# Optimization experiments

Hardware: AMD Instinct MI355X
Metric: run time of the kernel (lower is better)

## Reference

```python
import jax, jax.numpy as jnp
import numpy as np

B = 4096   # batch
I = 1024   # in_features
O = 1024   # out_features
N = 4      # LUT fan-in; table size 2**N = 16


def setup_inputs() -> dict:
    key = jax.random.key(0)
    k1, k2, k3 = jax.random.split(key, 3)
    return {
        "x": jax.random.normal(k1, (B, I), dtype=jnp.float32),
        # learnable mapping logits: (out_features, n, in_features)
        "mapping_logits": jax.random.normal(k2, (O, N, I), dtype=jnp.float32),
        # per-node LUT tables with 2**n corner values each
        "lut_tables": jax.random.normal(k3, (O, 2 ** N), dtype=jnp.float32),
    }


def reference(x, mapping_logits, lut_tables):
    # softmax-weighted input selection: (B,I) x (O,N,I) -> (B,O,N)
    w = jax.nn.softmax(mapping_logits, axis=-1)
    selected = jnp.einsum('bi,oni->bon', x, w)
    # BatchedLUTNodes: squash to [0,1], multilinear interpolation over 2**N corners
    s = jax.nn.sigmoid(selected)                      # (B,O,N)
    cw = jnp.ones(s.shape[:2] + (1,), dtype=s.dtype)  # corner weights, grows to (B,O,2**N)
    for j in range(N):                                # fixed small loop over fan-in
        sj = s[..., j][..., None]                     # (B,O,1)
        cw = jnp.concatenate([cw * (1.0 - sj), cw * sj], axis=-1)
    # weighted sum of per-node table entries -> (B,O)
    return jnp.einsum('boc,oc->bo', cw, lut_tables)
```

## Files before the change

kernel.cpp:

```cpp
#include <hip/hip_runtime.h>

#define B_DIM 4096
#define I_DIM 1024
#define O_DIM 1024
#define ON_DIM 4096
#define TILE_HALFS 4096

typedef _Float16 half8  __attribute__((ext_vector_type(8)));
typedef _Float16 half4_t __attribute__((ext_vector_type(4)));
typedef float    floatx4 __attribute__((ext_vector_type(4)));

__global__ __launch_bounds__(256)
void ltn_stats(const float* __restrict__ logits, float2* __restrict__ stats) {
  const int t = threadIdx.x, lane = t & 63, wv = t >> 6;
  const int row = blockIdx.x * 4 + wv;
  const float4* src = (const float4*)(logits + (size_t)row * I_DIM);
  float4 v[4];
#pragma unroll
  for (int j = 0; j < 4; j++) v[j] = src[j * 64 + lane];
  float m = -1e30f;
#pragma unroll
  for (int j = 0; j < 4; j++)
    m = fmaxf(m, fmaxf(fmaxf(v[j].x, v[j].y), fmaxf(v[j].z, v[j].w)));
#pragma unroll
  for (int off = 1; off < 64; off <<= 1) m = fmaxf(m, __shfl_xor(m, off));
  float s = 0.0f;
#pragma unroll
  for (int j = 0; j < 4; j++) {
    s += __expf(v[j].x - m) + __expf(v[j].y - m)
       + __expf(v[j].z - m) + __expf(v[j].w - m);
  }
#pragma unroll
  for (int off = 1; off < 64; off <<= 1) s += __shfl_xor(s, off);
  if (lane == 0) stats[row] = make_float2(m, 1.0f / s);
}

__global__ __launch_bounds__(256)
void ltn_tile(const float* __restrict__ logits, const float* __restrict__ x,
              const float2* __restrict__ stats,
              _Float16* __restrict__ wt, _Float16* __restrict__ xt) {
  const int t  = threadIdx.x;
  const int nn = t >> 1;
  const int hf = t & 1;
  if (blockIdx.x < 1024) {
    const int nb = blockIdx.x >> 5, kb = blockIdx.x & 31;
    const int row = nb * 128 + nn;
    const float2 st = stats[row];
    const float4* src = (const float4*)(logits + (size_t)row * I_DIM + kb * 32 + hf * 16);
    const float4 a = src[0], b = src[1], c = src[2], d = src[3];
    half8 h0, h1;
    h0[0] = (_Float16)(__expf(a.x - st.x) * st.y);
    h0[1] = (_Float16)(__expf(a.y - st.x) * st.y);
    h0[2] = (_Float16)(__expf(a.z - st.x) * st.y);
    h0[3] = (_Float16)(__expf(a.w - st.x) * st.y);
    h0[4] = (_Float16)(__expf(b.x - st.x) * st.y);
    h0[5] = (_Float16)(__expf(b.y - st.x) * st.y);
    h0[6] = (_Float16)(__expf(b.z - st.x) * st.y);
    h0[7] = (_Float16)(__expf(b.w - st.x) * st.y);
    h1[0] = (_Float16)(__expf(c.x - st.x) * st.y);
    h1[1] = (_Float16)(__expf(c.y - st.x) * st.y);
    h1[2] = (_Float16)(__expf(c.z - st.x) * st.y);
    h1[3] = (_Float16)(__expf(c.w - st.x) * st.y);
    h1[4] = (_Float16)(__expf(d.x - st.x) * st.y);
    h1[5] = (_Float16)(__expf(d.y - st.x) * st.y);
    h1[6] = (_Float16)(__expf(d.z - st.x) * st.y);
    h1[7] = (_Float16)(__expf(d.w - st.x) * st.y);
    _Float16* base = wt + ((size_t)nb * 32 + kb) * TILE_HALFS + (hf * 2) * 1024 + nn * 8;
    *(half8*)base = h0;
    *(half8*)(base + 1024) = h1;
  } else {
    const int bid = blockIdx.x - 1024;
    const int mb = bid >> 5, kt = bid & 31;
    const int row = mb * 128 + nn;
    const float4* src = (const float4*)(x + (size_t)row * I_DIM + kt * 32 + hf * 16);
    const float4 a = src[0], b = src[1], c = src[2], d = src[3];
    half8 h0, h1;
    h0[0] = (_Float16)a.x; h0[1] = (_Float16)a.y; h0[2] = (_Float16)a.z; h0[3] = (_Float16)a.w;
    h0[4] = (_Float16)b.x; h0[5] = (_Float16)b.y; h0[6] = (_Float16)b.z; h0[7] = (_Float16)b.w;
    h1[0] = (_Float16)c.x; h1[1] = (_Float16)c.y; h1[2] = (_Float16)c.z; h1[3] = (_Float16)c.w;
    h1[4] = (_Float16)d.x; h1[5] = (_Float16)d.y; h1[6] = (_Float16)d.z; h1[7] = (_Float16)d.w;
    _Float16* base = xt + ((size_t)mb * 32 + kt) * TILE_HALFS + (hf * 2) * 1024 + nn * 8;
    *(half8*)base = h0;
    *(half8*)(base + 1024) = h1;
  }
}

__global__ __launch_bounds__(512, 2)
void ltn_gemm_lut(const _Float16* __restrict__ xt,
                  const _Float16* __restrict__ wt,
                  const float* __restrict__ lut,
                  float* __restrict__ out) {
  __shared__ _Float16 As[2][2][4][128][8];
  __shared__ _Float16 Bs[2][2][4][128][8];

  const int tid  = threadIdx.x;
  const int lane = tid & 63;
  const int wv   = tid >> 6;
  const int wr   = wv >> 1;
  const int wc   = wv & 1;
  const int mb   = blockIdx.x;
  const int nb   = blockIdx.y;
  const int fm   = lane & 15;
  const int kq   = lane >> 4;

  const size_t baseA = (size_t)(mb * 2) * 32 * TILE_HALFS;
  const size_t baseB = (size_t)(nb * 2) * 32 * TILE_HALFS;

  floatx4 acc[4][8];
#pragma unroll
  for (int i = 0; i < 4; i++)
#pragma unroll
    for (int j = 0; j < 8; j++) acc[i][j] = (floatx4)0.0f;

  auto stage = [&](int buf, int kt) {
#pragma unroll
    for (int s = 0; s < 4; s++) {
      const int c   = wv * 4 + s;
      const int cc  = c & 15;
      const int tl  = cc >> 3;
      const int sub = cc & 7;
      const _Float16* g;
      char* l;
      if (c < 16) {
        g = xt + baseA + (size_t)(tl * 32 + kt) * TILE_HALFS + sub * 512 + lane * 8;
        l = (char*)&As[buf][0][0][0][0] + cc * 1024;
      } else {
        g = wt + baseB + (size_t)(tl * 32 + kt) * TILE_HALFS + sub * 512 + lane * 8;
        l = (char*)&Bs[buf][0][0][0][0] + cc * 1024;
      }
      __builtin_amdgcn_global_load_lds(
          (const __attribute__((address_space(1))) void*)g,
          (__attribute__((address_space(3))) void*)l, 16, 0, 0);
    }
  };

  auto compute = [&](int buf) {
    half8 af[4], bf[8];
#pragma unroll
    for (int f = 0; f < 4; f++)
      af[f] = *(const half8*)&As[buf][wr >> 1][kq][(wr & 1) * 64 + f * 16 + fm][0];
#pragma unroll
    for (int g = 0; g < 8; g++)
      bf[g] = *(const half8*)&Bs[buf][wc][kq][g * 16 + fm][0];
#pragma unroll
    for (int mt = 0; mt < 4; mt++)
#pragma unroll
      for (int nt = 0; nt < 8; nt++)
        acc[mt][nt] = __builtin_amdgcn_mfma_f32_16x16x32_f16(
            af[mt], bf[nt], acc[mt][nt], 0, 0, 0);
  };

  stage(0, 0);
  int buf = 0;
  for (int kt = 0; kt < 32; kt++) {
    __syncthreads();
    if (kt + 1 < 32) stage(buf ^ 1, kt + 1);
    compute(buf);
    buf ^= 1;
  }

#pragma unroll
  for (int nt = 0; nt < 8; nt++) {
    const int o = (nb * 256 + wc * 128 + nt * 16 + fm) >> 2;
    const float4* lt4 = (const float4*)(lut + (size_t)o * 16);
    const float4 L0 = lt4[0], L1 = lt4[1], L2 = lt4[2], L3 = lt4[3];
#pragma unroll
    for (int mt = 0; mt < 4; mt++) {
#pragma unroll
      for (int r = 0; r < 4; r++) {
        const float v  = acc[mt][nt][r];
        const float sv = 1.0f / (1.0f + __expf(-v));
        const float s1 = __shfl_down(sv, 1);
        const float s2 = __shfl_down(sv, 2);
        const float s3 = __shfl_down(sv, 3);
        if ((lane & 3) == 0) {
          const float s0 = sv;
          const float a0 = L0.x + (L2.x - L0.x) * s3;
          const float a1 = L0.y + (L2.y - L0.y) * s3;
          const float a2 = L0.z + (L2.z - L0.z) * s3;
          const float a3 = L0.w + (L2.w - L0.w) * s3;
          const float a4 = L1.x + (L3.x - L1.x) * s3;
          const float a5 = L1.y + (L3.y - L1.y) * s3;
          const float a6 = L1.z + (L3.z - L1.z) * s3;
          const float a7 = L1.w + (L3.w - L1.w) * s3;
          const float b0 = a0 + (a4 - a0) * s2;
          const float b1 = a1 + (a5 - a1) * s2;
          const float b2 = a2 + (a6 - a2) * s2;
          const float b3 = a3 + (a7 - a3) * s2;
          const float c0 = b0 + (b2 - b0) * s1;
          const float c1 = b1 + (b3 - b1) * s1;
          const float res = c0 + (c1 - c0) * s0;
          const int row = mb * 256 + wr * 64 + mt * 16 + (lane >> 4) * 4 + r;
          out[(size_t)row * O_DIM + o] = res;
        }
      }
    }
  }
}

extern "C" void kernel_launch(void* const* d_in, const int* in_sizes, int n_in,
                              void* d_out, int out_size, void* d_ws, size_t ws_size,
                              hipStream_t stream) {
  const float* x      = (const float*)d_in[0];
  const float* logits = (const float*)d_in[1];
  const float* lut    = (const float*)d_in[2];
  float* out          = (float*)d_out;

  _Float16* wt = (_Float16*)d_ws;
  _Float16* xt = (_Float16*)d_ws + (size_t)ON_DIM * I_DIM;
  float2* stats = (float2*)d_out;

  ltn_stats<<<1024, 256, 0, stream>>>(logits, stats);
  ltn_tile<<<2048, 256, 0, stream>>>(logits, x, stats, wt, xt);
  dim3 grid(16, 16);
  ltn_gemm_lut<<<grid, 512, 0, stream>>>(xt, wt, lut, out);
}
```

Before: 134.2 us.

## Triple-buffer GEMM LDS pipeline with vmcnt waits and XCD-aware block remap

```diff
diff --git a/kernel.cpp b/kernel.cpp
--- a/kernel.cpp
+++ b/kernel.cpp
@@ -90,18 +90,22 @@
                   const _Float16* __restrict__ wt,
                   const float* __restrict__ lut,
                   float* __restrict__ out) {
-  __shared__ _Float16 As[2][2][4][128][8];
-  __shared__ _Float16 Bs[2][2][4][128][8];
+  __shared__ _Float16 sm[3 * 16384];
 
   const int tid  = threadIdx.x;
   const int lane = tid & 63;
   const int wv   = tid >> 6;
   const int wr   = wv >> 1;
   const int wc   = wv & 1;
-  const int mb   = blockIdx.x;
-  const int nb   = blockIdx.y;
-  const int fm   = lane & 15;
-  const int kq   = lane >> 4;
+
+  const int id  = blockIdx.x;
+  const int xcd = id & 7;
+  const int li  = id >> 3;
+  const int mb  = (xcd & 3) * 4 + (li & 3);
+  const int nb  = (xcd >> 2) * 8 + (li >> 2);
+
+  const int fm = lane & 15;
+  const int kq = lane >> 4;
 
   const size_t baseA = (size_t)(mb * 2) * 32 * TILE_HALFS;
   const size_t baseB = (size_t)(nb * 2) * 32 * TILE_HALFS;
@@ -112,7 +116,7 @@
 #pragma unroll
     for (int j = 0; j < 8; j++) acc[i][j] = (floatx4)0.0f;
 
-  auto stage = [&](int buf, int kt) {
+  auto stage = [&](int bufOff , int kt) {
 #pragma unroll
     for (int s = 0; s < 4; s++) {
       const int c   = wv * 4 + s;
@@ -120,43 +124,52 @@
       const int tl  = cc >> 3;
       const int sub = cc & 7;
       const _Float16* g;
-      char* l;
+      int dst;
       if (c < 16) {
         g = xt + baseA + (size_t)(tl * 32 + kt) * TILE_HALFS + sub * 512 + lane * 8;
-        l = (char*)&As[buf][0][0][0][0] + cc * 1024;
+        dst = bufOff + cc * 512;
       } else {
         g = wt + baseB + (size_t)(tl * 32 + kt) * TILE_HALFS + sub * 512 + lane * 8;
-        l = (char*)&Bs[buf][0][0][0][0] + cc * 1024;
+        dst = bufOff + 8192 + cc * 512;
       }
       __builtin_amdgcn_global_load_lds(
           (const __attribute__((address_space(1))) void*)g,
-          (__attribute__((address_space(3))) void*)l, 16, 0, 0);
+          (__attribute__((address_space(3))) void*)(sm + dst), 16, 0, 0);
     }
   };
 
-  auto compute = [&](int buf) {
+  auto compute = [&](int bufOff) {
     half8 af[4], bf[8];
 #pragma unroll
     for (int f = 0; f < 4; f++)
-      af[f] = *(const half8*)&As[buf][wr >> 1][kq][(wr & 1) * 64 + f * 16 + fm][0];
+      af[f] = *(const half8*)&sm[bufOff + ((wr >> 1) * 4 + kq) * 1024
+                                 + ((wr & 1) * 64 + f * 16 + fm) * 8];
 #pragma unroll
     for (int g = 0; g < 8; g++)
-      bf[g] = *(const half8*)&Bs[buf][wc][kq][g * 16 + fm][0];
+      bf[g] = *(const half8*)&sm[bufOff + 8192 + (wc * 4 + kq) * 1024
+                                 + (g * 16 + fm) * 8];
+    __builtin_amdgcn_s_setprio(1);
 #pragma unroll
     for (int mt = 0; mt < 4; mt++)
 #pragma unroll
       for (int nt = 0; nt < 8; nt++)
         acc[mt][nt] = __builtin_amdgcn_mfma_f32_16x16x32_f16(
             af[mt], bf[nt], acc[mt][nt], 0, 0, 0);
+    __builtin_amdgcn_s_setprio(0);
   };
 
   stage(0, 0);
-  int buf = 0;
+  stage(16384, 1);
+  int o0 = 0, o1 = 16384, o2 = 32768;
+
   for (int kt = 0; kt < 32; kt++) {
-    __syncthreads();
-    if (kt + 1 < 32) stage(buf ^ 1, kt + 1);
-    compute(buf);
-    buf ^= 1;
+    if (kt < 31) asm volatile("s_waitcnt vmcnt(4)" ::: "memory");
+    else         asm volatile("s_waitcnt vmcnt(0)" ::: "memory");
+    __builtin_amdgcn_s_barrier();
+    __builtin_amdgcn_sched_barrier(0);
+    if (kt + 2 < 32) stage(o2, kt + 2);
+    compute(o0);
+    const int t0 = o0; o0 = o1; o1 = o2; o2 = t0;
   }
 
 #pragma unroll
@@ -212,6 +225,5 @@
 
   ltn_stats<<<1024, 256, 0, stream>>>(logits, stats);
   ltn_tile<<<2048, 256, 0, stream>>>(logits, x, stats, wt, xt);
-  dim3 grid(16, 16);
-  ltn_gemm_lut<<<grid, 512, 0, stream>>>(xt, wt, lut, out);
-}
+  ltn_gemm_lut<<<256, 512, 0, stream>>>(xt, wt, lut, out);
+}
```

After: 132.4 us. No clear change (-1.3%).

## Shrink GEMM block tile to 128x128 with XCD-aware block swizzle

Applied to the files above, without the earlier changes.

```diff
diff --git a/kernel.cpp b/kernel.cpp
--- a/kernel.cpp
+++ b/kernel.cpp
@@ -85,48 +85,50 @@
   }
 }
 
-__global__ __launch_bounds__(512, 2)
+__global__ __launch_bounds__(256, 4)
 void ltn_gemm_lut(const _Float16* __restrict__ xt,
                   const _Float16* __restrict__ wt,
                   const float* __restrict__ lut,
                   float* __restrict__ out) {
-  __shared__ _Float16 As[2][2][4][128][8];
-  __shared__ _Float16 Bs[2][2][4][128][8];
+  __shared__ _Float16 As[2][4][128][8];
+  __shared__ _Float16 Bs[2][4][128][8];
 
   const int tid  = threadIdx.x;
   const int lane = tid & 63;
   const int wv   = tid >> 6;
   const int wr   = wv >> 1;
   const int wc   = wv & 1;
-  const int mb   = blockIdx.x;
-  const int nb   = blockIdx.y;
-  const int fm   = lane & 15;
-  const int kq   = lane >> 4;
-
-  const size_t baseA = (size_t)(mb * 2) * 32 * TILE_HALFS;
-  const size_t baseB = (size_t)(nb * 2) * 32 * TILE_HALFS;
-
-  floatx4 acc[4][8];
+
+  const int id  = blockIdx.x;
+  const int xcd = id & 7;
+  const int li  = id >> 3;
+  const int mb  = (xcd & 3) * 8 + (li & 7);
+  const int nb  = (xcd >> 2) * 16 + (li >> 3);
+
+  const int fm = lane & 15;
+  const int kq = lane >> 4;
+
+  const size_t baseA = (size_t)mb * 32 * TILE_HALFS;
+  const size_t baseB = (size_t)nb * 32 * TILE_HALFS;
+
+  floatx4 acc[4][4];
 #pragma unroll
   for (int i = 0; i < 4; i++)
 #pragma unroll
-    for (int j = 0; j < 8; j++) acc[i][j] = (floatx4)0.0f;
+    for (int j = 0; j < 4; j++) acc[i][j] = (floatx4)0.0f;
 
   auto stage = [&](int buf, int kt) {
 #pragma unroll
     for (int s = 0; s < 4; s++) {
-      const int c   = wv * 4 + s;
-      const int cc  = c & 15;
-      const int tl  = cc >> 3;
-      const int sub = cc & 7;
+      const int c = wv * 4 + s;
       const _Float16* g;
       char* l;
-      if (c < 16) {
-        g = xt + baseA + (size_t)(tl * 32 + kt) * TILE_HALFS + sub * 512 + lane * 8;
-        l = (char*)&As[buf][0][0][0][0] + cc * 1024;
+      if (c < 8) {
+        g = xt + baseA + (size_t)kt * TILE_HALFS + c * 512 + lane * 8;
+        l = (char*)&As[buf][0][0][0] + c * 1024;
       } else {
-        g = wt + baseB + (size_t)(tl * 32 + kt) * TILE_HALFS + sub * 512 + lane * 8;
-        l = (char*)&Bs[buf][0][0][0][0] + cc * 1024;
+        g = wt + baseB + (size_t)kt * TILE_HALFS + (c - 8) * 512 + lane * 8;
+        l = (char*)&Bs[buf][0][0][0] + (c - 8) * 1024;
       }
       __builtin_amdgcn_global_load_lds(
           (const __attribute__((address_space(1))) void*)g,
@@ -135,23 +137,24 @@
   };
 
   auto compute = [&](int buf) {
-    half8 af[4], bf[8];
+    half8 af[4], bf[4];
 #pragma unroll
     for (int f = 0; f < 4; f++)
-      af[f] = *(const half8*)&As[buf][wr >> 1][kq][(wr & 1) * 64 + f * 16 + fm][0];
-#pragma unroll
-    for (int g = 0; g < 8; g++)
-      bf[g] = *(const half8*)&Bs[buf][wc][kq][g * 16 + fm][0];
+      af[f] = *(const half8*)&As[buf][kq][wr * 64 + f * 16 + fm][0];
+#pragma unroll
+    for (int g = 0; g < 4; g++)
+      bf[g] = *(const half8*)&Bs[buf][kq][wc * 64 + g * 16 + fm][0];
 #pragma unroll
     for (int mt = 0; mt < 4; mt++)
 #pragma unroll
-      for (int nt = 0; nt < 8; nt++)
+      for (int nt = 0; nt < 4; nt++)
         acc[mt][nt] = __builtin_amdgcn_mfma_f32_16x16x32_f16(
             af[mt], bf[nt], acc[mt][nt], 0, 0, 0);
   };
 
   stage(0, 0);
   int buf = 0;
+#pragma unroll 1
   for (int kt = 0; kt < 32; kt++) {
     __syncthreads();
     if (kt + 1 < 32) stage(buf ^ 1, kt + 1);
@@ -160,8 +163,8 @@
   }
 
 #pragma unroll
-  for (int nt = 0; nt < 8; nt++) {
-    const int o = (nb * 256 + wc * 128 + nt * 16 + fm) >> 2;
+  for (int nt = 0; nt < 4; nt++) {
+    const int o = (nb * 128 + wc * 64 + nt * 16 + fm) >> 2;
     const float4* lt4 = (const float4*)(lut + (size_t)o * 16);
     const float4 L0 = lt4[0], L1 = lt4[1], L2 = lt4[2], L3 = lt4[3];
 #pragma unroll
@@ -190,7 +193,7 @@
           const float c0 = b0 + (b2 - b0) * s1;
           const float c1 = b1 + (b3 - b1) * s1;
           const float res = c0 + (c1 - c0) * s0;
-          const int row = mb * 256 + wr * 64 + mt * 16 + (lane >> 4) * 4 + r;
+          const int row = mb * 128 + wr * 64 + mt * 16 + (lane >> 4) * 4 + r;
           out[(size_t)row * O_DIM + o] = res;
         }
       }
@@ -212,6 +215,5 @@
 
   ltn_stats<<<1024, 256, 0, stream>>>(logits, stats);
   ltn_tile<<<2048, 256, 0, stream>>>(logits, x, stats, wt, xt);
-  dim3 grid(16, 16);
-  ltn_gemm_lut<<<grid, 512, 0, stream>>>(xt, wt, lut, out);
-}
+  ltn_gemm_lut<<<1024, 256, 0, stream>>>(xt, wt, lut, out);
+}
```

After: 132.8 us. No clear change (-1.0%).
